# Optimization experiments

Measured on AMD Instinct MI355X. Metric: run time of the kernel, lower is better.

## Reference

```python
import jax, jax.numpy as jnp
import numpy as np

VAR_NUM = 96
EMBED_TIME = 128
INPUT_DIM = VAR_NUM * 2 + EMBED_TIME  # 320
ATTN_DIM = 64
N_HEADS = 8
ALL_DIM = ATTN_DIM * N_HEADS  # 512
B, N = 8, 2048
NEG_INF = -1e9  # finite stand-in for masked_fill(-inf); safe under softmax


def setup_inputs() -> dict:
    key = jax.random.key(0)
    ks = jax.random.split(key, 16)
    s = lambda d: 1.0 / np.sqrt(d)
    return {
        "times_in": jax.random.uniform(ks[0], (B, N), jnp.float32),
        "data_in": jax.random.normal(ks[1], (B, N, VAR_NUM), jnp.float32),
        "mask_in": jnp.ones((B, N, VAR_NUM), jnp.float32),
        "exist_times": jax.random.randint(ks[2], (B, N), 0, 2, jnp.int32),
        # TimeEmbedding params
        "w_per": jax.random.normal(ks[3], (1, EMBED_TIME - 1), jnp.float32),
        "b_per": jnp.zeros((EMBED_TIME - 1,), jnp.float32),
        "w_lin": jax.random.normal(ks[4], (1, 1), jnp.float32),
        "b_lin": jnp.zeros((1,), jnp.float32),
        # Attention params
        "Wq": jax.random.normal(ks[5], (INPUT_DIM, ALL_DIM), jnp.float32) * s(INPUT_DIM),
        "bq": jnp.zeros((ALL_DIM,), jnp.float32),
        "Wk": jax.random.normal(ks[6], (INPUT_DIM, ALL_DIM), jnp.float32) * s(INPUT_DIM),
        "bk": jnp.zeros((ALL_DIM,), jnp.float32),
        "Wv": jax.random.normal(ks[7], (INPUT_DIM, ALL_DIM), jnp.float32) * s(INPUT_DIM),
        "bv": jnp.zeros((ALL_DIM,), jnp.float32),
        "Wfc": jax.random.normal(ks[8], (ALL_DIM, ATTN_DIM), jnp.float32) * s(ALL_DIM),
        "bfc": jnp.zeros((ATTN_DIM,), jnp.float32),
    }


def reference(times_in, data_in, mask_in, exist_times,
              w_per, b_per, w_lin, b_lin,
              Wq, bq, Wk, bk, Wv, bv, Wfc, bfc):
    b, n = times_in.shape
    tt = times_in[..., None]  # [b, n, 1]
    # TimeEmbedding: [linear(tt), sin(periodic(tt))]
    te = jnp.concatenate([tt @ w_lin + b_lin, jnp.sin(tt @ w_per + b_per)], axis=-1)
    x = jnp.concatenate([data_in, mask_in, te], axis=-1)  # [b, n, INPUT_DIM]

    def heads(w, bias):
        return (x @ w + bias).reshape(b, n, N_HEADS, ATTN_DIM).transpose(0, 2, 1, 3)

    q, k, v = heads(Wq, bq), heads(Wk, bk), heads(Wv, bv)  # [b, h, n, d]
    # NOTE: custom scale uses sqrt(input_dim), not sqrt(head_dim)
    scores = jnp.einsum("bhqd,bhkd->bhqk", q, k) / jnp.sqrt(jnp.float32(INPUT_DIM))
    m = (exist_times != 0)
    scores = jnp.where(m[:, None, None, :], scores, NEG_INF)  # mask keys
    attn = jax.nn.softmax(scores, axis=-1)  # dropout p=0 in eval reference
    out = jnp.einsum("bhqk,bhkd->bhqd", attn, v)
    out = jnp.where(m[:, None, :, None], out, 0.0)  # zero masked query rows
    out = out.transpose(0, 2, 1, 3).reshape(b, n, ALL_DIM)
    return out @ Wfc + bfc  # [b, n, ATTN_DIM]
```

## Files before the change

### kernel.cpp

```cpp
#include <hip/hip_runtime.h>

#define N_ 2048
#define BN 16384
#define IN_DIM 320
#define QKV_N 1536
#define ALPHA 0.08064911f

typedef float f32x4 __attribute__((ext_vector_type(4)));
typedef short v8s __attribute__((ext_vector_type(8)));
typedef unsigned int u32x2 __attribute__((ext_vector_type(2)));

__device__ __forceinline__ short f2b(float f) {
  unsigned u = __builtin_bit_cast(unsigned, f);
  u = u + 0x7fff + ((u >> 16) & 1);
  return (short)(u >> 16);
}

__device__ __forceinline__ int piperm(int t) {
  return ((t >> 5) & 1) * 32 + ((t >> 2) & 3) * 8 + ((t >> 4) & 1) * 4 + (t & 3);
}

__global__ void build_x(const float* __restrict__ times, const float* __restrict__ data,
                        const float* __restrict__ maskv, const float* __restrict__ w_per,
                        const float* __restrict__ b_per, const float* __restrict__ w_lin,
                        const float* __restrict__ b_lin, short* __restrict__ x) {
  int row = blockIdx.x;
  int t = threadIdx.x;
  float tt = times[row];
  short* xr = x + (size_t)row * IN_DIM;
  const float* dr = data + (size_t)row * 96;
  const float* mr = maskv + (size_t)row * 96;
  if (t < 96) { xr[t] = f2b(dr[t]); xr[96 + t] = f2b(mr[t]); }
  float val;
  if (t == 0) val = tt * w_lin[0] + b_lin[0];
  else        val = __sinf(tt * w_per[t - 1] + b_per[t - 1]);
  xr[192 + t] = f2b(val);
}

__global__ void scan_mask(const int* __restrict__ exist, int* __restrict__ prefix,
                          int* __restrict__ ntg, int* __restrict__ totals,
                          short* __restrict__ flagsc) {
  __shared__ int sums[256];
  int b = blockIdx.x;
  int t = threadIdx.x;
  const int* e = exist + b * 2048;
  int loc[8];
  int s = 0;
#pragma unroll
  for (int j = 0; j < 8; ++j) { loc[j] = s; s += (e[t * 8 + j] != 0) ? 1 : 0; }
  sums[t] = s;
  __syncthreads();
  for (int d = 1; d < 256; d <<= 1) {
    int v = (t >= d) ? sums[t - d] : 0;
    __syncthreads();
    sums[t] += v;
    __syncthreads();
  }
  int total = sums[255];
  int base = (t == 0) ? 0 : sums[t - 1];
#pragma unroll
  for (int j = 0; j < 8; ++j) prefix[b * 2048 + t * 8 + j] = base + loc[j];
  if (t == 0) { ntg[b] = (total + 63) >> 6; totals[b] = total; }
#pragma unroll
  for (int j = 0; j < 8; ++j) {
    int slot = t * 8 + j;
    flagsc[b * 2048 + (slot & ~63) + piperm(slot & 63)] =
        (slot < total) ? (short)0x3F80 : (short)0;
  }
}

__global__ void zero_pad(const int* __restrict__ ntg, const int* __restrict__ totals,
                         short* __restrict__ kc) {
  int bh = blockIdx.x;
  int b = bh >> 3;
  int nt = ntg[b], total = totals[b];
  int pad = nt * 64 - total;
  int t = threadIdx.x;
  v8s z = {0, 0, 0, 0, 0, 0, 0, 0};
  for (int i = t; i < pad * 8; i += 512)
    *(v8s*)&kc[((size_t)bh * N_ + total) * 64 + i * 8] = z;
}

__global__ void transpose_w(const float* __restrict__ Wq, const float* __restrict__ Wk,
                            const float* __restrict__ Wv, const float* __restrict__ Wfc,
                            short* __restrict__ Wt, short* __restrict__ WfcT) {
  int idx = blockIdx.x * 256 + threadIdx.x;
  if (idx < QKV_N * IN_DIM) {
    int n = idx / IN_DIM, kk = idx - n * IN_DIM;
    const float* W = (n < 512) ? Wq : (n < 1024 ? Wk : Wv);
    Wt[idx] = f2b(W[(size_t)kk * 512 + (n & 511)]);
  } else {
    int j = idx - QKV_N * IN_DIM;
    int d = j >> 9, kk = j & 511;
    WfcT[j] = f2b(Wfc[kk * 64 + d]);
  }
}

__launch_bounds__(256)
__global__ void qkv_gemm(const short* __restrict__ x, const short* __restrict__ Wt,
                         const float* __restrict__ bq, const float* __restrict__ bk,
                         const float* __restrict__ bv, const int* __restrict__ exist,
                         const int* __restrict__ prefix,
                         short* __restrict__ q, short* __restrict__ kc, short* __restrict__ vc) {
  __shared__ short As[128][40];
  __shared__ short Bs[128][40];
  int bm = blockIdx.x;
  int bn = blockIdx.y;
  int tid = threadIdx.x, wave = tid >> 6, lane = tid & 63;
  int wm = wave >> 1, wn = wave & 1;
  int l16 = lane & 15, lh = lane >> 4;
  f32x4 acc[4][4] = {};
  for (int kt = 0; kt < 10; ++kt) {
    int k0 = kt * 32;
#pragma unroll
    for (int s = 0; s < 2; ++s) {
      int c = tid + s * 256;
      int r = c >> 2, c8 = c & 3;
      *(v8s*)&As[r][c8 * 8] = *(const v8s*)&x[(size_t)(bm * 128 + r) * IN_DIM + k0 + c8 * 8];
      *(v8s*)&Bs[r][c8 * 8] = *(const v8s*)&Wt[(size_t)(bn * 128 + r) * IN_DIM + k0 + c8 * 8];
    }
    __syncthreads();
    v8s af[4], bfr[4];
#pragma unroll
    for (int m = 0; m < 4; ++m) af[m] = *(const v8s*)&As[wm * 64 + m * 16 + l16][lh * 8];
#pragma unroll
    for (int n = 0; n < 4; ++n) bfr[n] = *(const v8s*)&Bs[wn * 64 + n * 16 + l16][lh * 8];
#pragma unroll
    for (int m = 0; m < 4; ++m)
#pragma unroll
      for (int n = 0; n < 4; ++n)
        acc[m][n] = __builtin_amdgcn_mfma_f32_16x16x32_bf16(af[m], bfr[n], acc[m][n], 0, 0, 0);
    __syncthreads();
  }
  int w = bn >> 2;
  if (w == 0) {
#pragma unroll
    for (int m = 0; m < 4; ++m) {
      int row0 = bm * 128 + wm * 64 + m * 16 + lh * 4;
#pragma unroll
      for (int n = 0; n < 4; ++n) {
        int c = (bn * 128 + wn * 64 + n * 16 + l16) & 511;
        float bb = bq[c];
        int h = c >> 6, d = c & 63;
#pragma unroll
        for (int r = 0; r < 4; ++r) {
          int rr = row0 + r;
          int b = rr >> 11, ntok = rr & 2047;
          q[(((size_t)(b * 8 + h) * N_ + ntok) << 6) + d] = f2b((acc[m][n][r] + bb) * ALPHA);
        }
      }
    }
  } else {
    short* dbuf = (w == 1) ? kc : vc;
    const float* bias = (w == 1) ? bk : bv;
#pragma unroll
    for (int m = 0; m < 4; ++m) {
      int row0 = bm * 128 + wm * 64 + m * 16 + lh * 4;
      int exr[4], dstr[4];
#pragma unroll
      for (int r = 0; r < 4; ++r) { exr[r] = exist[row0 + r]; dstr[r] = prefix[row0 + r]; }
      int b = row0 >> 11;
#pragma unroll
      for (int n = 0; n < 4; ++n) {
        int c = (bn * 128 + wn * 64 + n * 16 + l16) & 511;
        float bb = bias[c];
        int h = c >> 6, d = c & 63;
#pragma unroll
        for (int r = 0; r < 4; ++r)
          if (exr[r])
            dbuf[(((size_t)(b * 8 + h) * N_ + dstr[r]) << 6) + d] = f2b(acc[m][n][r] + bb);
      }
    }
  }
}

__launch_bounds__(256)
__global__ void fragmentize(const short* __restrict__ vc, const int* __restrict__ ntg,
                            const int* __restrict__ totals, short* __restrict__ vT) {
  __shared__ short Vs[64][66];
  int bh = blockIdx.x;
  int b = bh >> 3;
  int nt = ntg[b], total = totals[b];
  int tid = threadIdx.x;
  const short* vcp = vc + (size_t)bh * N_ * 64;
  short* vtp = vT + (size_t)bh * 131072;
  for (int tile = blockIdx.y; tile < nt; tile += 4) {
    int base = tile * 64;
#pragma unroll
    for (int s = 0; s < 2; ++s) {
      int c = tid + s * 256, r = c >> 3, c8 = c & 7;
      v8s val = {0, 0, 0, 0, 0, 0, 0, 0};
      if (base + r < total) val = *(const v8s*)&vcp[(size_t)(base + r) * 64 + c8 * 8];
      *(v8s*)&Vs[r][c8 * 8] = val;
    }
    __syncthreads();
#pragma unroll
    for (int s = 0; s < 2; ++s) {
      int c = tid + s * 256;
      int l16 = c & 15, lh = (c >> 4) & 3, kc2 = (c >> 6) & 1, n2 = c >> 7;
      int d = n2 * 16 + l16;
      v8s o;
#pragma unroll
      for (int jj = 0; jj < 8; ++jj) {
        int t2 = kc2 * 32 + (jj >> 2) * 16 + lh * 4 + (jj & 3);
        o[jj] = Vs[t2][d];
      }
      *(v8s*)&vtp[(size_t)tile * 4096 + c * 8] = o;
    }
    __syncthreads();
  }
}

__launch_bounds__(256, 2)
__global__ void attn_kernel(const short* __restrict__ q, const short* __restrict__ kc,
                            const short* __restrict__ vT, const short* __restrict__ flagsc,
                            const int* __restrict__ ntg, const int* __restrict__ exist,
                            short* __restrict__ att) {
  int bx = blockIdx.x;
  int bh = ((bx >> 6) << 3) | (bx & 7);
  int qblk = (bx >> 3) & 7;
  int b = bh >> 3, h = bh & 7;
  int tid = threadIdx.x, wave = tid >> 6, lane = tid & 63;
  int l16 = lane & 15, lh = lane >> 4;
  int q0 = qblk * 256 + wave * 64;
  int nt = ntg[b];
  const short* qp = q + (size_t)bh * N_ * 64;
  const short* kcp = kc + (size_t)bh * N_ * 64;
  const short* vpt = vT + (size_t)bh * 131072;
  const short* fpt = flagsc + b * N_;
  const int* ex = exist + b * N_;
  v8s qf[4][2];
#pragma unroll
  for (int m = 0; m < 4; ++m)
#pragma unroll
    for (int kcx = 0; kcx < 2; ++kcx)
      qf[m][kcx] = *(const v8s*)&qp[(size_t)(q0 + m * 16 + l16) * 64 + kcx * 32 + lh * 8];
  f32x4 oacc[4][4] = {};
  f32x4 lacc[4] = {};
  const f32x4 zf = {0.f, 0.f, 0.f, 0.f};
  int voff = lane * 8;
  int vok = l16 * 64 + lh * 8;
  v8s kf[8], vf[8], ff[2];
#pragma unroll
  for (int i = 0; i < 8; ++i) {
    kf[i] = *(const v8s*)&kcp[(i >> 1) * 1024 + (i & 1) * 32 + vok];
    vf[i] = *(const v8s*)&vpt[i * 512 + voff];
  }
  ff[0] = *(const v8s*)&fpt[lh * 8];
  ff[1] = *(const v8s*)&fpt[32 + lh * 8];
#pragma unroll 1
  for (int kt = 0; kt < nt; ++kt) {
    const short* kn = kcp + (size_t)(kt + 1) * 4096;
    const short* vn = vpt + (size_t)(kt + 1) * 4096;
    const short* fn = fpt + (kt + 1) * 64;
    bool pre = (kt + 1 < nt);
#pragma unroll
    for (int mh = 0; mh < 2; ++mh) {
      f32x4 sacc[2][4];
#pragma unroll
      for (int n = 0; n < 4; ++n)
#pragma unroll
        for (int mm = 0; mm < 2; ++mm) {
          sacc[mm][n] = __builtin_amdgcn_mfma_f32_16x16x32_bf16(kf[n * 2], qf[mh * 2 + mm][0], zf, 0, 0, 0);
          sacc[mm][n] = __builtin_amdgcn_mfma_f32_16x16x32_bf16(kf[n * 2 + 1], qf[mh * 2 + mm][1], sacc[mm][n], 0, 0, 0);
        }
      if (mh == 1 && pre)
#pragma unroll
        for (int i = 0; i < 8; ++i)
          kf[i] = *(const v8s*)&kn[(i >> 1) * 1024 + (i & 1) * 32 + vok];
      v8s pf[2][2];
#pragma unroll
      for (int mm = 0; mm < 2; ++mm)
#pragma unroll
        for (int kcx = 0; kcx < 2; ++kcx)
#pragma unroll
          for (int half = 0; half < 2; ++half) {
            int n = kcx * 2 + half;
            float p0 = __builtin_amdgcn_exp2f(sacc[mm][n][0]);
            float p1 = __builtin_amdgcn_exp2f(sacc[mm][n][1]);
            float p2 = __builtin_amdgcn_exp2f(sacc[mm][n][2]);
            float p3 = __builtin_amdgcn_exp2f(sacc[mm][n][3]);
            uint w0, w1;
            asm("v_cvt_pk_bf16_f32 %0, %1, %2" : "=v"(w0) : "v"(p0), "v"(p1));
            asm("v_cvt_pk_bf16_f32 %0, %1, %2" : "=v"(w1) : "v"(p2), "v"(p3));
            ((uint*)&pf[mm][kcx])[half * 2]     = w0;
            ((uint*)&pf[mm][kcx])[half * 2 + 1] = w1;
          }
#pragma unroll
      for (int kcx = 0; kcx < 2; ++kcx) {
#pragma unroll
        for (int mm = 0; mm < 2; ++mm)
          lacc[mh * 2 + mm] = __builtin_amdgcn_mfma_f32_16x16x32_bf16(pf[mm][kcx], ff[kcx], lacc[mh * 2 + mm], 0, 0, 0);
#pragma unroll
        for (int n = 0; n < 4; ++n)
#pragma unroll
          for (int mm = 0; mm < 2; ++mm)
            oacc[mh * 2 + mm][n] = __builtin_amdgcn_mfma_f32_16x16x32_bf16(pf[mm][kcx], vf[n * 2 + kcx], oacc[mh * 2 + mm][n], 0, 0, 0);
      }
    }
    if (pre) {
#pragma unroll
      for (int i = 0; i < 8; ++i) vf[i] = *(const v8s*)&vn[i * 512 + voff];
      ff[0] = *(const v8s*)&fn[lh * 8];
      ff[1] = *(const v8s*)&fn[32 + lh * 8];
    }
  }
#pragma unroll
  for (int m = 0; m < 4; ++m)
#pragma unroll
    for (int r = 0; r < 4; ++r) {
      int row = q0 + m * 16 + lh * 4 + r;
      float qm = (ex[row] != 0) ? 1.f : 0.f;
      float inv = qm / fmaxf(lacc[m][r], 1e-20f);
#pragma unroll
      for (int n = 0; n < 4; ++n)
        att[((size_t)(b * N_ + row)) * 512 + h * 64 + n * 16 + l16] = f2b(oacc[m][n][r] * inv);
    }
}

__launch_bounds__(256)
__global__ void out_gemm(const short* __restrict__ att, const short* __restrict__ WfcT,
                         const float* __restrict__ bfc, float* __restrict__ out) {
  __shared__ short As[128][40];
  __shared__ short Bs[64][40];
  int bm = blockIdx.x;
  int tid = threadIdx.x, wave = tid >> 6, lane = tid & 63;
  int l16 = lane & 15, lh = lane >> 4;
  f32x4 acc[2][4] = {};
  for (int kt = 0; kt < 16; ++kt) {
    int k0 = kt * 32;
#pragma unroll
    for (int s = 0; s < 2; ++s) {
      int c = tid + s * 256;
      int r = c >> 2, c8 = c & 3;
      *(v8s*)&As[r][c8 * 8] = *(const v8s*)&att[(size_t)(bm * 128 + r) * 512 + k0 + c8 * 8];
    }
    { int r = tid >> 2, c8 = tid & 3;
      if (r < 64) *(v8s*)&Bs[r][c8 * 8] = *(const v8s*)&WfcT[(size_t)r * 512 + k0 + c8 * 8]; }
    __syncthreads();
    v8s bfr[4];
#pragma unroll
    for (int n = 0; n < 4; ++n) bfr[n] = *(const v8s*)&Bs[n * 16 + l16][lh * 8];
#pragma unroll
    for (int m = 0; m < 2; ++m) {
      v8s af = *(const v8s*)&As[wave * 32 + m * 16 + l16][lh * 8];
#pragma unroll
      for (int n = 0; n < 4; ++n)
        acc[m][n] = __builtin_amdgcn_mfma_f32_16x16x32_bf16(af, bfr[n], acc[m][n], 0, 0, 0);
    }
    __syncthreads();
  }
#pragma unroll
  for (int m = 0; m < 2; ++m)
#pragma unroll
    for (int n = 0; n < 4; ++n) {
      float bb = bfc[n * 16 + l16];
#pragma unroll
      for (int r = 0; r < 4; ++r) {
        int row = bm * 128 + wave * 32 + m * 16 + lh * 4 + r;
        out[(size_t)row * 64 + n * 16 + l16] = acc[m][n][r] + bb;
      }
    }
}

extern "C" void kernel_launch(void* const* d_in, const int* in_sizes, int n_in,
                              void* d_out, int out_size, void* d_ws, size_t ws_size,
                              hipStream_t stream) {
  const float* times = (const float*)d_in[0];
  const float* data  = (const float*)d_in[1];
  const float* maskv = (const float*)d_in[2];
  const int*   exist = (const int*)d_in[3];
  const float* w_per = (const float*)d_in[4];
  const float* b_per = (const float*)d_in[5];
  const float* w_lin = (const float*)d_in[6];
  const float* b_lin = (const float*)d_in[7];
  const float* Wq  = (const float*)d_in[8];
  const float* bq  = (const float*)d_in[9];
  const float* Wk  = (const float*)d_in[10];
  const float* bk  = (const float*)d_in[11];
  const float* Wv  = (const float*)d_in[12];
  const float* bv  = (const float*)d_in[13];
  const float* Wfc = (const float*)d_in[14];
  const float* bfc = (const float*)d_in[15];
  float* out = (float*)d_out;

  char* ws = (char*)d_ws;
  short* x     = (short*)(ws);
  short* Wt    = (short*)(ws + 10485760);
  short* WfcT  = (short*)(ws + 11468800);
  short* qb    = (short*)(ws + 11534336);
  short* kcb   = (short*)(ws + 28311552);
  short* vTb   = (short*)(ws + 45088768);
  short* vcb   = (short*)(ws + 61865984);
  short* att   = (short*)(ws + 61865984);
  short* flagsc= (short*)(ws + 78643200);
  int*   prefix= (int*)(ws + 78675968);
  int*   ntg   = (int*)(ws + 78741504);
  int*   totals= (int*)(ws + 78741536);

  build_x<<<BN, 128, 0, stream>>>(times, data, maskv, w_per, b_per, w_lin, b_lin, x);
  scan_mask<<<8, 256, 0, stream>>>(exist, prefix, ntg, totals, flagsc);
  transpose_w<<<2048, 256, 0, stream>>>(Wq, Wk, Wv, Wfc, Wt, WfcT);
  qkv_gemm<<<dim3(128, 12), 256, 0, stream>>>(x, Wt, bq, bk, bv, exist, prefix, qb, kcb, vcb);
  zero_pad<<<64, 512, 0, stream>>>(ntg, totals, kcb);
  fragmentize<<<dim3(64, 4), 256, 0, stream>>>(vcb, ntg, totals, vTb);
  attn_kernel<<<512, 256, 0, stream>>>(qb, kcb, vTb, flagsc, ntg, exist, att);
  out_gemm<<<128, 256, 0, stream>>>(att, WfcT, bfc, out);
}
```

Baseline: 126.8 us.

## Pre-fragment K in place alongside V and drop the zero_pad kernel

The fragmentize kernel now rearranges both the compacted K and V buffers in place into per-lane MFMA fragment order, zero-filling padded rows as it goes. This replaces the separate zero_pad launch. The attention kernel can then load K with contiguous lane*8 offsets instead of strided row gathers. The fragmentize grid doubles in y to cover the extra work, and the separate vT buffer is removed. The cost is extra LDS traffic and work in fragmentize, plus reliance on each block rewriting only the tile it read.

```diff
diff --git a/kernel.cpp b/kernel.cpp
--- a/kernel.cpp
+++ b/kernel.cpp
@@ -67,18 +67,6 @@
     flagsc[b * 2048 + (slot & ~63) + piperm(slot & 63)] =
         (slot < total) ? (short)0x3F80 : (short)0;
   }
-}
-
-__global__ void zero_pad(const int* __restrict__ ntg, const int* __restrict__ totals,
-                         short* __restrict__ kc) {
-  int bh = blockIdx.x;
-  int b = bh >> 3;
-  int nt = ntg[b], total = totals[b];
-  int pad = nt * 64 - total;
-  int t = threadIdx.x;
-  v8s z = {0, 0, 0, 0, 0, 0, 0, 0};
-  for (int i = t; i < pad * 8; i += 512)
-    *(v8s*)&kc[((size_t)bh * N_ + total) * 64 + i * 8] = z;
 }
 
 __global__ void transpose_w(const float* __restrict__ Wq, const float* __restrict__ Wk,
@@ -175,28 +163,36 @@
 }
 
 __launch_bounds__(256)
-__global__ void fragmentize(const short* __restrict__ vc, const int* __restrict__ ntg,
-                            const int* __restrict__ totals, short* __restrict__ vT) {
+__global__ void fragmentize(short* __restrict__ kc, short* __restrict__ vc,
+                            const int* __restrict__ ntg, const int* __restrict__ totals) {
+  __shared__ short Ks[64][66];
   __shared__ short Vs[64][66];
   int bh = blockIdx.x;
   int b = bh >> 3;
   int nt = ntg[b], total = totals[b];
   int tid = threadIdx.x;
-  const short* vcp = vc + (size_t)bh * N_ * 64;
-  short* vtp = vT + (size_t)bh * 131072;
-  for (int tile = blockIdx.y; tile < nt; tile += 4) {
+  size_t hb = (size_t)bh * N_ * 64;
+  for (int tile = blockIdx.y; tile < nt; tile += 8) {
     int base = tile * 64;
 #pragma unroll
     for (int s = 0; s < 2; ++s) {
       int c = tid + s * 256, r = c >> 3, c8 = c & 7;
-      v8s val = {0, 0, 0, 0, 0, 0, 0, 0};
-      if (base + r < total) val = *(const v8s*)&vcp[(size_t)(base + r) * 64 + c8 * 8];
-      *(v8s*)&Vs[r][c8 * 8] = val;
+      v8s kv = {0, 0, 0, 0, 0, 0, 0, 0};
+      v8s vv = {0, 0, 0, 0, 0, 0, 0, 0};
+      if (base + r < total) {
+        kv = *(const v8s*)&kc[hb + (size_t)(base + r) * 64 + c8 * 8];
+        vv = *(const v8s*)&vc[hb + (size_t)(base + r) * 64 + c8 * 8];
+      }
+      *(v8s*)&Ks[r][c8 * 8] = kv;
+      *(v8s*)&Vs[r][c8 * 8] = vv;
     }
     __syncthreads();
 #pragma unroll
     for (int s = 0; s < 2; ++s) {
       int c = tid + s * 256;
+      int i = c >> 6, lh2 = (c >> 4) & 3, r16 = c & 15;
+      *(v8s*)&kc[hb + (size_t)tile * 4096 + c * 8] =
+          *(const v8s*)&Ks[(i >> 1) * 16 + r16][(i & 1) * 32 + lh2 * 8];
       int l16 = c & 15, lh = (c >> 4) & 3, kc2 = (c >> 6) & 1, n2 = c >> 7;
       int d = n2 * 16 + l16;
       v8s o;
@@ -205,14 +201,14 @@
         int t2 = kc2 * 32 + (jj >> 2) * 16 + lh * 4 + (jj & 3);
         o[jj] = Vs[t2][d];
       }
-      *(v8s*)&vtp[(size_t)tile * 4096 + c * 8] = o;
+      *(v8s*)&vc[hb + (size_t)tile * 4096 + c * 8] = o;
     }
     __syncthreads();
   }
 }
 
 __launch_bounds__(256, 2)
-__global__ void attn_kernel(const short* __restrict__ q, const short* __restrict__ kc,
+__global__ void attn_kernel(const short* __restrict__ q, const short* __restrict__ kT,
                             const short* __restrict__ vT, const short* __restrict__ flagsc,
                             const int* __restrict__ ntg, const int* __restrict__ exist,
                             short* __restrict__ att) {
@@ -225,7 +221,7 @@
   int q0 = qblk * 256 + wave * 64;
   int nt = ntg[b];
   const short* qp = q + (size_t)bh * N_ * 64;
-  const short* kcp = kc + (size_t)bh * N_ * 64;
+  const short* kpt = kT + (size_t)bh * 131072;
   const short* vpt = vT + (size_t)bh * 131072;
   const short* fpt = flagsc + b * N_;
   const int* ex = exist + b * N_;
@@ -239,18 +235,17 @@
   f32x4 lacc[4] = {};
   const f32x4 zf = {0.f, 0.f, 0.f, 0.f};
   int voff = lane * 8;
-  int vok = l16 * 64 + lh * 8;
   v8s kf[8], vf[8], ff[2];
 #pragma unroll
   for (int i = 0; i < 8; ++i) {
-    kf[i] = *(const v8s*)&kcp[(i >> 1) * 1024 + (i & 1) * 32 + vok];
+    kf[i] = *(const v8s*)&kpt[i * 512 + voff];
     vf[i] = *(const v8s*)&vpt[i * 512 + voff];
   }
   ff[0] = *(const v8s*)&fpt[lh * 8];
   ff[1] = *(const v8s*)&fpt[32 + lh * 8];
 #pragma unroll 1
   for (int kt = 0; kt < nt; ++kt) {
-    const short* kn = kcp + (size_t)(kt + 1) * 4096;
+    const short* kn = kpt + (size_t)(kt + 1) * 4096;
     const short* vn = vpt + (size_t)(kt + 1) * 4096;
     const short* fn = fpt + (kt + 1) * 64;
     bool pre = (kt + 1 < nt);
@@ -266,8 +261,7 @@
         }
       if (mh == 1 && pre)
 #pragma unroll
-        for (int i = 0; i < 8; ++i)
-          kf[i] = *(const v8s*)&kn[(i >> 1) * 1024 + (i & 1) * 32 + vok];
+        for (int i = 0; i < 8; ++i) kf[i] = *(const v8s*)&kn[i * 512 + voff];
       v8s pf[2][2];
 #pragma unroll
       for (int mm = 0; mm < 2; ++mm)
@@ -390,8 +384,7 @@
   short* WfcT  = (short*)(ws + 11468800);
   short* qb    = (short*)(ws + 11534336);
   short* kcb   = (short*)(ws + 28311552);
-  short* vTb   = (short*)(ws + 45088768);
-  short* vcb   = (short*)(ws + 61865984);
+  short* vcb   = (short*)(ws + 45088768);
   short* att   = (short*)(ws + 61865984);
   short* flagsc= (short*)(ws + 78643200);
   int*   prefix= (int*)(ws + 78675968);
@@ -402,8 +395,7 @@
   scan_mask<<<8, 256, 0, stream>>>(exist, prefix, ntg, totals, flagsc);
   transpose_w<<<2048, 256, 0, stream>>>(Wq, Wk, Wv, Wfc, Wt, WfcT);
   qkv_gemm<<<dim3(128, 12), 256, 0, stream>>>(x, Wt, bq, bk, bv, exist, prefix, qb, kcb, vcb);
-  zero_pad<<<64, 512, 0, stream>>>(ntg, totals, kcb);
-  fragmentize<<<dim3(64, 4), 256, 0, stream>>>(vcb, ntg, totals, vTb);
-  attn_kernel<<<512, 256, 0, stream>>>(qb, kcb, vTb, flagsc, ntg, exist, att);
+  fragmentize<<<dim3(64, 8), 256, 0, stream>>>(kcb, vcb, ntg, totals);
+  attn_kernel<<<512, 256, 0, stream>>>(qb, kcb, vcb, flagsc, ntg, exist, att);
   out_gemm<<<128, 256, 0, stream>>>(att, WfcT, bfc, out);
 }
```

New measurement: 111.6 us. 1.14x faster.
